# Performance work log

Hardware: AMD Instinct MI355X
Metric: run time of the kernel (lower is better)

## Reference

```python
import jax, jax.numpy as jnp
import numpy as np

MIN_VAL = 0.0
MAX_VAL = 1.0
NUM_BINS = 512
NUM_NODES = 128
GRAD_SMOOTH = 0.01
BIN_W = (MAX_VAL - MIN_VAL) / NUM_BINS


def _make_kernels():
    sobel = jnp.array([-1.0, 0.0, 1.0], dtype=jnp.float32) / (2.0 * BIN_W)
    r = max(1, int(GRAD_SMOOTH / BIN_W))  # kernel radius in bins
    idx = jnp.arange(2 * r + 1, dtype=jnp.float32) - r
    sigma = GRAD_SMOOTH / BIN_W
    g = jnp.exp(-0.5 * (idx / sigma) ** 2)
    return sobel, g / jnp.sum(g)


def _conv1d_reflect(x, k):
    # x: [N, B], k: [K]; torch Conv1d = cross-correlation with reflect padding
    pad = (k.shape[0] - 1) // 2
    xp = jnp.pad(x, ((0, 0), (pad, pad)), mode='reflect')
    out = jax.lax.conv_general_dilated(
        xp[:, None, :], k[None, None, :], (1,), 'VALID',
        dimension_numbers=('NCH', 'OIH', 'NCH'))
    return out[:, 0, :]


def _compute_cdf_pdf(residuals, weights, src_indices, dst_indices):
    # histogram bin per sample (floor)
    bi = jnp.floor((residuals - MIN_VAL) / BIN_W).astype(jnp.int32)
    valid = (bi >= 0) & (bi < NUM_BINS)
    bi = jnp.clip(bi, 0, NUM_BINS - 1)
    wc = (weights * valid).reshape(-1)  # [N_pairs*K]

    src_comb = (src_indices[:, None] * NUM_BINS + bi).reshape(-1)
    dst_comb = (dst_indices[:, None] * NUM_BINS + bi).reshape(-1)
    nseg = NUM_NODES * NUM_BINS
    hist = (jax.ops.segment_sum(wc, src_comb, num_segments=nseg)
            + jax.ops.segment_sum(wc, dst_comb, num_segments=nseg))
    hist = hist.reshape(NUM_NODES, NUM_BINS)

    wflat = weights.reshape(-1)
    src_exp = jnp.broadcast_to(src_indices[:, None], residuals.shape).reshape(-1)
    dst_exp = jnp.broadcast_to(dst_indices[:, None], residuals.shape).reshape(-1)
    tw = (jax.ops.segment_sum(wflat, src_exp, num_segments=NUM_NODES)
          + jax.ops.segment_sum(wflat, dst_exp, num_segments=NUM_NODES))

    pmf = hist / (tw[:, None] + 1e-10)
    cdf = jnp.cumsum(pmf, axis=1)
    sobel, gauss = _make_kernels()
    pdf = _conv1d_reflect(_conv1d_reflect(cdf, sobel), gauss)
    return cdf, pdf


def _lookup(residuals, weights, cdf, pdf, src_indices, dst_indices):
    # rounded bin for lookup (floor of x + 0.5)
    bi = jnp.floor((residuals - MIN_VAL) / BIN_W + 0.5).astype(jnp.int32)
    valid = (bi >= 0) & (bi < NUM_BINS) & (weights > 0.0)
    bi = jnp.clip(bi, 0, NUM_BINS - 1)
    src_cdf = cdf[src_indices[:, None], bi]
    dst_cdf = cdf[dst_indices[:, None], bi]
    src_grad = pdf[src_indices[:, None], bi] * weights
    dst_grad = pdf[dst_indices[:, None], bi] * weights
    two = jnp.float32(2.0)
    return (jnp.where(valid, src_cdf, two),
            jnp.where(valid, src_grad, 0.0),
            jnp.where(valid, dst_cdf, two),
            jnp.where(valid, dst_grad, 0.0))


def setup_inputs() -> dict:
    key = jax.random.key(0)
    k1, k2, k3, k4 = jax.random.split(key, 4)
    N_pairs, K = 1024, 16384
    return {
        'residuals': jax.random.uniform(k1, (N_pairs, K), dtype=jnp.float32),
        'weights': jax.random.uniform(k2, (N_pairs, K), dtype=jnp.float32),
        'src_indices': jax.random.randint(k3, (N_pairs,), 0, NUM_NODES),
        'dst_indices': jax.random.randint(k4, (N_pairs,), 0, NUM_NODES),
    }


def reference(residuals, weights, src_indices, dst_indices):
    cdf, pdf = _compute_cdf_pdf(residuals, weights, src_indices, dst_indices)
    src_cdf, _, dst_cdf, _ = _lookup(residuals, weights, cdf, pdf,
                                     src_indices, dst_indices)
    return src_cdf, dst_cdf
```

## Files before the change

kernel.cpp:

```cpp
#include <hip/hip_runtime.h>

#define NUM_BINS  512
#define NUM_NODES 128
#define K_ELEMS   16384
#define N_PAIRS   1024
#define NCOPY     32

typedef float f32x4 __attribute__((ext_vector_type(4)));
typedef float f32x2 __attribute__((ext_vector_type(2)));
typedef unsigned int   u32;
typedef unsigned short u16;

__device__ __forceinline__ void gfadd(float* p, float v) { unsafeAtomicAdd(p, v); }

__global__ __launch_bounds__(256) void zero_ws_kernel(float* __restrict__ ws, int n)
{
    int i = blockIdx.x * 256 + threadIdx.x;
    if (i < n) ws[i] = 0.0f;
}

__global__ __launch_bounds__(1024) void hist_kernel(
    const float* __restrict__ residuals, const float* __restrict__ weights,
    const int* __restrict__ src, const int* __restrict__ dst,
    float* __restrict__ hist, float* __restrict__ tw,
    u16* __restrict__ mask)
{
    __shared__ u32 lh[NUM_BINS * NCOPY];
    __shared__ float swsum[16];
    const int row  = blockIdx.x;
    const int t    = threadIdx.x;
    const int copy = t & 31;

    uint4* lh4 = (uint4*)lh;
    #pragma unroll
    for (int k = 0; k < NUM_BINS * NCOPY / 4 / 1024; ++k) {
        uint4 z; z.x = z.y = z.z = z.w = 0u;
        lh4[t + k * 1024] = z;
    }
    __syncthreads();

    const f32x4* r4 = (const f32x4*)(residuals + (size_t)row * K_ELEMS);
    const f32x4* w4 = (const f32x4*)(weights   + (size_t)row * K_ELEMS);

    float wsum = 0.0f;
    u32 vbits = 0;
    #pragma unroll
    for (int it = 0; it < K_ELEMS / 4 / 1024; ++it) {
        f32x4 r = r4[t + it * 1024];
        f32x4 w = __builtin_nontemporal_load(w4 + (t + it * 1024));
        wsum += w[0] + w[1] + w[2] + w[3];
        #pragma unroll
        for (int c = 0; c < 4; ++c) {
            int b = (int)floorf(r[c] * 512.0f);
            if ((unsigned)b < 512u)
                atomicAdd(&lh[b * NCOPY + copy], (u32)fmaf(w[c], 65536.0f, 0.5f));
            int lb = (int)floorf(r[c] * 512.0f + 0.5f);
            if (((unsigned)lb < 512u) & (w[c] > 0.0f))
                vbits |= 1u << (it * 4 + c);
        }
    }
    mask[(size_t)row * 1024 + t] = (u16)vbits;

    #pragma unroll
    for (int off = 32; off > 0; off >>= 1) wsum += __shfl_down(wsum, off, 64);
    const int wave = t >> 6, lane = t & 63;
    if (lane == 0) swsum[wave] = wsum;
    __syncthreads();

    const int s = src[row], d = dst[row];
    if (t == 0) {
        float tot = 0.0f;
        #pragma unroll
        for (int i = 0; i < 16; ++i) tot += swsum[i];
        gfadd(&tw[s], tot);
        gfadd(&tw[d], tot);
    }

    {
        const int bin  = t >> 1;
        const int half = t & 1;
        u32 tot = 0;
        #pragma unroll
        for (int cc = 0; cc < 16; ++cc)
            tot += lh[bin * NCOPY + (((bin + cc) & 15) | (half << 4))];
        tot += (u32)__shfl_xor((int)tot, 1);
        float v = (float)tot * (1.0f / 65536.0f);
        if (half == 0) gfadd(&hist[s * NUM_BINS + bin], v);
        else           gfadd(&hist[d * NUM_BINS + bin], v);
    }
}

__global__ __launch_bounds__(512) void lookup_scan_kernel(
    const float* __restrict__ residuals, const u16* __restrict__ mask,
    const int* __restrict__ src, const int* __restrict__ dst,
    const float* __restrict__ hist, const float* __restrict__ tw,
    float* __restrict__ out_src, float* __restrict__ out_dst)
{
    __shared__ f32x2 sd[NUM_BINS];
    const int row = blockIdx.x;
    const int t   = threadIdx.x;

    const int s = src[row], d = dst[row];
    {
        f32x2 v;
        v[0] = hist[s * NUM_BINS + t] / (tw[s] + 1e-10f);
        v[1] = hist[d * NUM_BINS + t] / (tw[d] + 1e-10f);
        sd[t] = v;
    }
    __syncthreads();

    for (int off = 1; off < NUM_BINS; off <<= 1) {
        f32x2 add = (t >= off) ? sd[t - off] : (f32x2){0.0f, 0.0f};
        __syncthreads();
        sd[t] += add;
        __syncthreads();
    }

    const size_t base = (size_t)row * K_ELEMS;
    const f32x4* r4   = (const f32x4*)(residuals + base);
    f32x4*       os4  = (f32x4*)(out_src + base);
    f32x4*       od4  = (f32x4*)(out_dst + base);

    const u32 m0 = mask[(size_t)row * 1024 + t];
    const u32 m1 = mask[(size_t)row * 1024 + t + 512];

    #pragma unroll
    for (int it = 0; it < K_ELEMS / 4 / 512; ++it) {
        const int q = t + it * 512;
        const u32 mw = (it & 1) ? m1 : m0;
        const int kb = (it >> 1) * 4;
        f32x4 r = r4[q];
        f32x4 osv, odv;
        #pragma unroll
        for (int c = 0; c < 4; ++c) {
            int lb = (int)floorf(r[c] * 512.0f + 0.5f);
            int bc = min(max(lb, 0), NUM_BINS - 1);
            bool v = (mw >> (kb + c)) & 1u;
            f32x2 vv = v ? sd[bc] : (f32x2){2.0f, 2.0f};
            osv[c] = vv[0]; odv[c] = vv[1];
        }
        __builtin_nontemporal_store(osv, os4 + q);
        __builtin_nontemporal_store(odv, od4 + q);
    }
}

extern "C" void kernel_launch(void* const* d_in, const int* in_sizes, int n_in,
                              void* d_out, int out_size, void* d_ws, size_t ws_size,
                              hipStream_t stream)
{
    const float* residuals = (const float*)d_in[0];
    const float* weights   = (const float*)d_in[1];
    const int*   src       = (const int*)d_in[2];
    const int*   dst       = (const int*)d_in[3];

    float* out_src = (float*)d_out;
    float* out_dst = out_src + (size_t)N_PAIRS * K_ELEMS;

    float* hist = (float*)d_ws;
    float* tw   = hist + NUM_NODES * NUM_BINS;
    u16*   mask = (u16*)((char*)d_ws + (4u << 20));

    const int ws_elems = NUM_NODES * NUM_BINS + NUM_NODES;
    zero_ws_kernel<<<(ws_elems + 255) / 256, 256, 0, stream>>>((float*)d_ws, ws_elems);

    hist_kernel<<<N_PAIRS, 1024, 0, stream>>>(residuals, weights, src, dst,
                                              hist, tw, mask);

    lookup_scan_kernel<<<N_PAIRS, 512, 0, stream>>>(residuals, mask, src, dst,
                                                    hist, tw, out_src, out_dst);
}
```

Measured before the change: 66.68 us.

## Halve hist block size, prefetch loads, and hoist lookup residual loads above scan

The histogram kernel now runs 512 threads per block with 16 LDS histogram copies instead of 32, so each block needs half the shared memory. It software-pipelines the residual and weight loads one iteration ahead and packs the validity mask into 32-bit words. The lookup kernel issues all eight residual vector loads and the mask load before the shared-memory prefix scan, so global memory latency overlaps the scan. The cost is more LDS atomic contention per copy and higher register pressure from holding the prefetched vectors.

```diff
diff --git a/kernel.cpp b/kernel.cpp
--- a/kernel.cpp
+++ b/kernel.cpp
@@ -4,7 +4,7 @@
 #define NUM_NODES 128
 #define K_ELEMS   16384
 #define N_PAIRS   1024
-#define NCOPY     32
+#define NCOPY     16
 
 typedef float f32x4 __attribute__((ext_vector_type(4)));
 typedef float f32x2 __attribute__((ext_vector_type(2)));
@@ -19,23 +19,23 @@
     if (i < n) ws[i] = 0.0f;
 }
 
-__global__ __launch_bounds__(1024) void hist_kernel(
+__global__ __launch_bounds__(512) void hist_kernel(
     const float* __restrict__ residuals, const float* __restrict__ weights,
     const int* __restrict__ src, const int* __restrict__ dst,
     float* __restrict__ hist, float* __restrict__ tw,
-    u16* __restrict__ mask)
+    u32* __restrict__ mask)
 {
     __shared__ u32 lh[NUM_BINS * NCOPY];
-    __shared__ float swsum[16];
+    __shared__ float swsum[8];
     const int row  = blockIdx.x;
     const int t    = threadIdx.x;
-    const int copy = t & 31;
+    const int copy = t & 15;
 
     uint4* lh4 = (uint4*)lh;
     #pragma unroll
-    for (int k = 0; k < NUM_BINS * NCOPY / 4 / 1024; ++k) {
+    for (int k = 0; k < NUM_BINS * NCOPY / 4 / 512; ++k) {
         uint4 z; z.x = z.y = z.z = z.w = 0u;
-        lh4[t + k * 1024] = z;
+        lh4[t + k * 512] = z;
     }
     __syncthreads();
 
@@ -44,22 +44,29 @@
 
     float wsum = 0.0f;
     u32 vbits = 0;
+
+    f32x4 rA = r4[t];
+    f32x4 wA = __builtin_nontemporal_load(w4 + t);
     #pragma unroll
-    for (int it = 0; it < K_ELEMS / 4 / 1024; ++it) {
-        f32x4 r = r4[t + it * 1024];
-        f32x4 w = __builtin_nontemporal_load(w4 + (t + it * 1024));
-        wsum += w[0] + w[1] + w[2] + w[3];
+    for (int it = 0; it < K_ELEMS / 4 / 512; ++it) {
+        f32x4 rB, wB;
+        if (it < K_ELEMS / 4 / 512 - 1) {
+            rB = r4[t + (it + 1) * 512];
+            wB = __builtin_nontemporal_load(w4 + (t + (it + 1) * 512));
+        }
+        wsum += wA[0] + wA[1] + wA[2] + wA[3];
         #pragma unroll
         for (int c = 0; c < 4; ++c) {
-            int b = (int)floorf(r[c] * 512.0f);
+            int b = (int)floorf(rA[c] * 512.0f);
             if ((unsigned)b < 512u)
-                atomicAdd(&lh[b * NCOPY + copy], (u32)fmaf(w[c], 65536.0f, 0.5f));
-            int lb = (int)floorf(r[c] * 512.0f + 0.5f);
-            if (((unsigned)lb < 512u) & (w[c] > 0.0f))
+                atomicAdd(&lh[b * NCOPY + copy], (u32)fmaf(wA[c], 65536.0f, 0.5f));
+            int lb = (int)floorf(rA[c] * 512.0f + 0.5f);
+            if (((unsigned)lb < 512u) & (wA[c] > 0.0f))
                 vbits |= 1u << (it * 4 + c);
         }
+        rA = rB; wA = wB;
     }
-    mask[(size_t)row * 1024 + t] = (u16)vbits;
+    mask[(size_t)row * 512 + t] = vbits;
 
     #pragma unroll
     for (int off = 32; off > 0; off >>= 1) wsum += __shfl_down(wsum, off, 64);
@@ -71,27 +78,24 @@
     if (t == 0) {
         float tot = 0.0f;
         #pragma unroll
-        for (int i = 0; i < 16; ++i) tot += swsum[i];
+        for (int i = 0; i < 8; ++i) tot += swsum[i];
         gfadd(&tw[s], tot);
         gfadd(&tw[d], tot);
     }
 
     {
-        const int bin  = t >> 1;
-        const int half = t & 1;
         u32 tot = 0;
         #pragma unroll
-        for (int cc = 0; cc < 16; ++cc)
-            tot += lh[bin * NCOPY + (((bin + cc) & 15) | (half << 4))];
-        tot += (u32)__shfl_xor((int)tot, 1);
+        for (int cc = 0; cc < NCOPY; ++cc)
+            tot += lh[t * NCOPY + ((t + cc) & 15)];
         float v = (float)tot * (1.0f / 65536.0f);
-        if (half == 0) gfadd(&hist[s * NUM_BINS + bin], v);
-        else           gfadd(&hist[d * NUM_BINS + bin], v);
+        gfadd(&hist[s * NUM_BINS + t], v);
+        gfadd(&hist[d * NUM_BINS + t], v);
     }
 }
 
 __global__ __launch_bounds__(512) void lookup_scan_kernel(
-    const float* __restrict__ residuals, const u16* __restrict__ mask,
+    const float* __restrict__ residuals, const u32* __restrict__ mask,
     const int* __restrict__ src, const int* __restrict__ dst,
     const float* __restrict__ hist, const float* __restrict__ tw,
     float* __restrict__ out_src, float* __restrict__ out_dst)
@@ -99,6 +103,15 @@
     __shared__ f32x2 sd[NUM_BINS];
     const int row = blockIdx.x;
     const int t   = threadIdx.x;
+
+    const size_t base = (size_t)row * K_ELEMS;
+    const f32x4* r4   = (const f32x4*)(residuals + base);
+
+    f32x4 rr0 = r4[t],           rr1 = r4[t + 512];
+    f32x4 rr2 = r4[t + 1024],    rr3 = r4[t + 1536];
+    f32x4 rr4 = r4[t + 2048],    rr5 = r4[t + 2560];
+    f32x4 rr6 = r4[t + 3072],    rr7 = r4[t + 3584];
+    const u32 mw = mask[(size_t)row * 512 + t];
 
     const int s = src[row], d = dst[row];
     {
@@ -116,32 +129,26 @@
         __syncthreads();
     }
 
-    const size_t base = (size_t)row * K_ELEMS;
-    const f32x4* r4   = (const f32x4*)(residuals + base);
-    f32x4*       os4  = (f32x4*)(out_src + base);
-    f32x4*       od4  = (f32x4*)(out_dst + base);
+    f32x4* os4 = (f32x4*)(out_src + base);
+    f32x4* od4 = (f32x4*)(out_dst + base);
 
-    const u32 m0 = mask[(size_t)row * 1024 + t];
-    const u32 m1 = mask[(size_t)row * 1024 + t + 512];
-
-    #pragma unroll
-    for (int it = 0; it < K_ELEMS / 4 / 512; ++it) {
-        const int q = t + it * 512;
-        const u32 mw = (it & 1) ? m1 : m0;
-        const int kb = (it >> 1) * 4;
-        f32x4 r = r4[q];
-        f32x4 osv, odv;
-        #pragma unroll
-        for (int c = 0; c < 4; ++c) {
-            int lb = (int)floorf(r[c] * 512.0f + 0.5f);
-            int bc = min(max(lb, 0), NUM_BINS - 1);
-            bool v = (mw >> (kb + c)) & 1u;
-            f32x2 vv = v ? sd[bc] : (f32x2){2.0f, 2.0f};
-            osv[c] = vv[0]; odv[c] = vv[1];
-        }
-        __builtin_nontemporal_store(osv, os4 + q);
-        __builtin_nontemporal_store(odv, od4 + q);
+    #define EMIT(IT, RV)                                                       \
+    {                                                                          \
+        f32x4 osv, odv;                                                        \
+        _Pragma("unroll")                                                      \
+        for (int c = 0; c < 4; ++c) {                                          \
+            int lb = (int)floorf(RV[c] * 512.0f + 0.5f);                       \
+            int bc = min(max(lb, 0), NUM_BINS - 1);                            \
+            bool v = (mw >> (IT * 4 + c)) & 1u;                                \
+            f32x2 vv = v ? sd[bc] : (f32x2){2.0f, 2.0f};                       \
+            osv[c] = vv[0]; odv[c] = vv[1];                                    \
+        }                                                                      \
+        __builtin_nontemporal_store(osv, os4 + (t + IT * 512));                \
+        __builtin_nontemporal_store(odv, od4 + (t + IT * 512));                \
     }
+    EMIT(0, rr0) EMIT(1, rr1) EMIT(2, rr2) EMIT(3, rr3)
+    EMIT(4, rr4) EMIT(5, rr5) EMIT(6, rr6) EMIT(7, rr7)
+    #undef EMIT
 }
 
 extern "C" void kernel_launch(void* const* d_in, const int* in_sizes, int n_in,
@@ -158,13 +165,13 @@
 
     float* hist = (float*)d_ws;
     float* tw   = hist + NUM_NODES * NUM_BINS;
-    u16*   mask = (u16*)((char*)d_ws + (4u << 20));
+    u32*   mask = (u32*)((char*)d_ws + (4u << 20));
 
     const int ws_elems = NUM_NODES * NUM_BINS + NUM_NODES;
     zero_ws_kernel<<<(ws_elems + 255) / 256, 256, 0, stream>>>((float*)d_ws, ws_elems);
 
-    hist_kernel<<<N_PAIRS, 1024, 0, stream>>>(residuals, weights, src, dst,
-                                              hist, tw, mask);
+    hist_kernel<<<N_PAIRS, 512, 0, stream>>>(residuals, weights, src, dst,
+                                             hist, tw, mask);
 
     lookup_scan_kernel<<<N_PAIRS, 512, 0, stream>>>(residuals, mask, src, dst,
                                                     hist, tw, out_src, out_dst);
```

Measured after the change: 64.32 us, median of 2. -3.5%, faster.
